# Optimization experiments

Hardware: AMD Instinct MI355X
Metric: run time of the kernel (lower is better)

The kernel has to match this reference:

```python
import jax, jax.numpy as jnp
import numpy as np

B, L, H, NE, SPAN = 16, 2048, 768, 64, 4
EPS_COS = 1e-8   # torch cosine_similarity eps
EPS_STD = 1e-5   # std stabilizer from the module


def _linear_init(key, fan_in, fan_out):
    s = 1.0 / np.sqrt(fan_in)
    kw, kb = jax.random.split(key)
    w = jax.random.uniform(kw, (fan_in, fan_out), jnp.float32, -s, s)
    b = jax.random.uniform(kb, (fan_out,), jnp.float32, -s, s)
    return w, b


def setup_inputs() -> dict:
    key = jax.random.key(0)
    ks = jax.random.split(key, 6)
    w1, b1 = _linear_init(ks[0], 2 * H + 1, H)
    w2, b2 = _linear_init(ks[1], H, 512)
    w3, b3 = _linear_init(ks[2], 512, 256)
    w4, b4 = _linear_init(ks[3], 256, 2)
    x = jax.random.normal(ks[4], (B, L, H), jnp.float32)
    entity_starts = jax.random.randint(ks[5], (B, NE), 0, L - SPAN)
    threshold = jnp.float32(0.9)
    return dict(x=x, threshold=threshold,
                w1=w1, b1=b1, w2=w2, b2=b2, w3=w3, b3=b3, w4=w4, b4=b4,
                entity_starts=entity_starts)


def reference(x, threshold, w1, b1, w2, b2, w3, b3, w4, b4, entity_starts):
    # --- per-entity span max-pool (segment-max over x) ---
    # gather span tokens: [B, NE*SPAN] token indices into the L axis
    idx = (entity_starts[:, :, None] + jnp.arange(SPAN)).reshape(B, NE * SPAN)
    spans = jnp.take_along_axis(x, idx[:, :, None], axis=1)      # [B, NE*SPAN, H]
    emb = spans.reshape(B, NE, SPAN, H).max(axis=2)               # [B, NE, H]

    # --- pairwise cosine similarity per batch ---
    norm = jnp.maximum(jnp.linalg.norm(emb, axis=-1, keepdims=True), EPS_COS)
    n = emb / norm
    cos = jnp.einsum('bie,bje->bij', n, n)                        # [B, NE, NE]
    std = jnp.std(cos, axis=(1, 2), ddof=1, keepdims=True)        # torch .std() is unbiased
    sim = (cos - threshold) / (std + EPS_STD)
    sim = jnp.triu(sim, k=1)

    # --- all i<j pairs: [sim, emb_i, emb_j] ---
    iu, ju = np.triu_indices(NE, k=1)                             # static pair indices
    feats = jnp.concatenate(
        [sim[:, iu, ju, None], emb[:, iu, :], emb[:, ju, :]], axis=-1
    ).reshape(-1, 2 * H + 1)                                      # [B*P, 2H+1]

    # --- classifier MLP (dropout = identity at eval) ---
    h = jax.nn.relu(feats @ w1 + b1)
    h = jax.nn.relu(h @ w2 + b2)
    h = jax.nn.relu(h @ w3 + b3)
    logits = h @ w4 + b4                                          # [B*P, 2]
    return logits
```

## Files before the change

kernel.cpp:

```cpp
#include <hip/hip_runtime.h>
#include <cstdint>
#include <cstddef>

#define B_    16
#define L_    2048
#define H_    768
#define NE_   64
#define SPAN_ 4
#define NPAIR 2016
#define NROWS (B_ * NPAIR)

typedef __bf16 bf16_t;
typedef __bf16 bf16x8 __attribute__((ext_vector_type(8)));
typedef __bf16 bf16x4 __attribute__((ext_vector_type(4)));
typedef float  floatx4 __attribute__((ext_vector_type(4)));

#define AS1 __attribute__((address_space(1)))
#define AS3 __attribute__((address_space(3)))

#define OFF_EMBH   ((size_t)3145728)
#define OFF_NRMG   ((size_t)4718592)
#define OFF_SIM    ((size_t)8126464)
#define OFF_W1ABT  ((size_t)8255488)
#define OFF_W2T    ((size_t)10614784)
#define OFF_W3T    ((size_t)11401216)
#define OFF_C1     ((size_t)11663360)
#define OFF_H2     ((size_t)67500032)
#define OFF_FLAG   ((size_t)117045248)
#define OFF_CANON  ((size_t)117045504)

#define SWZ(colb, row) ((colb) ^ (((row) & 3) << 4))

__device__ inline bf16_t cvt_elem(const void* p, size_t i, int isf) {
  if (isf) return (bf16_t)(((const float*)p)[i]);
  return ((const bf16_t*)p)[i];
}

__global__ __launch_bounds__(1024) void prep_kernel(
    const unsigned short* __restrict__ xu,
    const void* __restrict__ xv, const int* __restrict__ starts,
    const void* __restrict__ w1, const void* __restrict__ w2,
    const void* __restrict__ w3, const void* __restrict__ b1,
    const void* __restrict__ b2, const void* __restrict__ b3,
    const void* __restrict__ w4, const void* __restrict__ b4,
    int* __restrict__ flagout,
    bf16_t* __restrict__ w1abT, bf16_t* __restrict__ w2T,
    bf16_t* __restrict__ w3T, bf16_t* __restrict__ canon,
    bf16_t* __restrict__ embh, bf16_t* __restrict__ nrm_g) {
  __shared__ bf16_t tile[64][65];
  __shared__ int tot[16];
  int blk = blockIdx.x;
  int t = threadIdx.x;

  {
    int bad = 0;
    for (int i = t; i < 4096; i += 1024) {
      int e = (xu[i] >> 7) & 0xFF;
      if (e > 133 || (e > 0 && e < 90)) bad++;
    }
    for (int off = 32; off > 0; off >>= 1) bad += __shfl_down(bad, off, 64);
    if ((t & 63) == 0) tot[t >> 6] = bad;
    __syncthreads();
  }
  int sumb = 0;
#pragma unroll
  for (int i = 0; i < 16; i++) sumb += tot[i];
  int isf = (sumb > 200) ? 1 : 0;
  __syncthreads();

  for (int u = blk; u < 481; u += 256) {
    if (u < 64) {
      int lane = t & 63;
      int entity = u * 16 + (t >> 6);
      int st = starts[entity];
      int b = entity >> 6;
      size_t off = ((size_t)(b * L_ + st)) * H_;
      int d0 = lane * 12;
      float pool[12];
      float ss = 0.f;
      if (isf) {
        const float* xp = (const float*)xv + off + d0;
#pragma unroll
        for (int k = 0; k < 3; k++) {
          floatx4 r0 = *(const floatx4*)(xp + k * 4);
          floatx4 r1 = *(const floatx4*)(xp + H_ + k * 4);
          floatx4 r2 = *(const floatx4*)(xp + 2 * H_ + k * 4);
          floatx4 r3 = *(const floatx4*)(xp + 3 * H_ + k * 4);
#pragma unroll
          for (int q = 0; q < 4; q++) {
            float v = fmaxf(fmaxf(r0[q], r1[q]), fmaxf(r2[q], r3[q]));
            pool[k * 4 + q] = v;
            ss += v * v;
          }
        }
      } else {
        const bf16_t* xp = (const bf16_t*)xv + off + d0;
#pragma unroll
        for (int k = 0; k < 3; k++) {
          bf16x4 r0 = *(const bf16x4*)(xp + k * 4);
          bf16x4 r1 = *(const bf16x4*)(xp + H_ + k * 4);
          bf16x4 r2 = *(const bf16x4*)(xp + 2 * H_ + k * 4);
          bf16x4 r3 = *(const bf16x4*)(xp + 3 * H_ + k * 4);
#pragma unroll
          for (int q = 0; q < 4; q++) {
            float v = fmaxf(fmaxf((float)r0[q], (float)r1[q]),
                            fmaxf((float)r2[q], (float)r3[q]));
            pool[k * 4 + q] = v;
            ss += v * v;
          }
        }
      }
#pragma unroll
      for (int d = 1; d < 64; d <<= 1) ss += __shfl_xor(ss, d, 64);
      float inv = 1.0f / fmaxf(sqrtf(ss), 1e-8f);
      size_t base = (size_t)entity * 768 + d0;
#pragma unroll
      for (int k = 0; k < 3; k++) {
        bf16x4 op, on;
#pragma unroll
        for (int q = 0; q < 4; q++) {
          op[q] = (bf16_t)pool[k * 4 + q];
          on[q] = (bf16_t)(pool[k * 4 + q] * inv);
        }
        *(bf16x4*)(embh + base + k * 4) = op;
        *(bf16x4*)(nrm_g + base + k * 4) = on;
      }
    } else if (u == 64) {
      if (t == 0) flagout[0] = isf;
      for (int idx = t; idx < 2818; idx += 1024) {
        if (idx < 768)       canon[idx] = cvt_elem(w1, idx, isf);
        else if (idx < 1536) canon[idx] = cvt_elem(b1, idx - 768, isf);
        else if (idx < 2048) canon[idx] = cvt_elem(b2, idx - 1536, isf);
        else if (idx < 2304) canon[idx] = cvt_elem(b3, idx - 2048, isf);
        else if (idx < 2816) canon[idx] = cvt_elem(w4, idx - 2304, isf);
        else                 canon[idx] = cvt_elem(b4, idx - 2816, isf);
      }
    } else {
      int tix = u - 65;
      const void* src; size_t srcoff; bf16_t* dst; int K, N;
      if (tix < 144)      { src = w1; srcoff = 768;               dst = w1abT;          K = 768; N = 768; }
      else if (tix < 288) { src = w1; srcoff = (size_t)769 * 768; dst = w1abT + 589824; K = 768; N = 768; tix -= 144; }
      else if (tix < 384) { src = w2; srcoff = 0;                 dst = w2T;            K = 768; N = 512; tix -= 288; }
      else                { src = w3; srcoff = 0;                 dst = w3T;            K = 512; N = 256; tix -= 384; }
      int tiles_k = K >> 6;
      int tn_t = tix / tiles_k, tk_t = tix - tn_t * tiles_k;
      int ty = t >> 6, tx = t & 63;
      __syncthreads();
#pragma unroll
      for (int p = 0; p < 4; p++) {
        int kk = tk_t * 64 + p * 16 + ty;
        int nn = tn_t * 64 + tx;
        tile[p * 16 + ty][tx] = cvt_elem(src, srcoff + (size_t)kk * N + nn, isf);
      }
      __syncthreads();
#pragma unroll
      for (int p = 0; p < 4; p++) {
        int nn = tn_t * 64 + p * 16 + ty;
        int kk = tk_t * 64 + tx;
        dst[(size_t)nn * K + kk] = tile[tx][p * 16 + ty];
      }
    }
  }
}

__global__ __launch_bounds__(256) void cosgemm1_kernel(
    const bf16_t* __restrict__ nrm_g, const bf16_t* __restrict__ embh,
    const bf16_t* __restrict__ w1abT, const int* __restrict__ flagp,
    const void* __restrict__ thr_ptr, float* __restrict__ simv,
    bf16_t* __restrict__ C1) {
  __shared__ __align__(16) char shb[98304];
  __shared__ float red1[4], red2[4];
  __shared__ float scale_s, thr_s;
  int blk = blockIdx.x;
  int t = threadIdx.x;
  int w = t >> 6, lane = t & 63;
  int quad = lane >> 4, l15 = lane & 15;

  if (blk < 16) {
    bf16_t* nrm = (bf16_t*)shb;
    int b = blk;
    const bf16_t* src = nrm_g + (size_t)b * 64 * 768;
    {
      int lr = t >> 2, c0 = (t & 3) * 192;
      for (int i = 0; i < 24; i++) {
        int col = c0 + i * 8;
        bf16x8 v = *(const bf16x8*)(src + lr * 768 + col);
        *(bf16x8*)((char*)nrm + ((lr * 1536 + col * 2) ^ ((lr & 7) << 4))) = v;
      }
    }
    __syncthreads();

    int rowA = w * 16 + l15;
    int xa = (rowA & 7) << 4;
    floatx4 acc[4] = {};
    for (int k0 = 0; k0 < 768; k0 += 32) {
      int cb = (k0 + quad * 8) * 2;
      bf16x8 aF = *(const bf16x8*)((char*)nrm + ((rowA * 1536 + cb) ^ xa));
#pragma unroll
      for (int tj = 0; tj < 4; tj++) {
        int rb = tj * 16 + l15;
        bf16x8 bF = *(const bf16x8*)((char*)nrm + ((rb * 1536 + cb) ^ ((rb & 7) << 4)));
        acc[tj] = __builtin_amdgcn_mfma_f32_16x16x32_bf16(aF, bF, acc[tj], 0, 0, 0);
      }
    }

    float s1 = 0.f, s2 = 0.f;
#pragma unroll
    for (int tj = 0; tj < 4; tj++)
#pragma unroll
      for (int r = 0; r < 4; r++) { s1 += acc[tj][r]; s2 += acc[tj][r] * acc[tj][r]; }
#pragma unroll
    for (int d = 1; d < 64; d <<= 1) {
      s1 += __shfl_xor(s1, d, 64);
      s2 += __shfl_xor(s2, d, 64);
    }
    if (lane == 0) { red1[w] = s1; red2[w] = s2; }
    __syncthreads();
    if (t == 0) {
      float S1 = red1[0] + red1[1] + red1[2] + red1[3];
      float S2 = red2[0] + red2[1] + red2[2] + red2[3];
      float mean = S1 * (1.0f / 4096.0f);
      float var = (S2 - 4096.0f * mean * mean) * (1.0f / 4095.0f);
      float sd = sqrtf(fmaxf(var, 0.f));
      scale_s = 1.0f / (sd + 1e-5f);
      thr_s = flagp[0] ? *(const float*)thr_ptr : (float)(*(const bf16_t*)thr_ptr);
    }
    __syncthreads();
    float sc = scale_s, th = thr_s;
#pragma unroll
    for (int tj = 0; tj < 4; tj++) {
      int j = tj * 16 + l15;
#pragma unroll
      for (int r = 0; r < 4; r++) {
        int i = w * 16 + quad * 4 + r;
        if (j > i) {
          int p = i * 63 - (i * (i - 1)) / 2 + (j - i - 1);
          simv[b * NPAIR + p] = (acc[tj][r] - th) * sc;
        }
      }
    }
    return;
  }

  const int K = 768, N = 1536;
  int bi = blk - 16;
  int bm = bi / 12, bn = bi - bm * 12;
  int wm = w >> 1, wn = w & 1;

  floatx4 acc[2][4] = {};
  const char* Abase = (const char*)(embh + (size_t)bm * 64 * K);
  const char* Bbase = (const char*)(w1abT + (size_t)bn * 128 * K);
  const int rowbytes = K * 2;

  {
    int fo = w * 1024 + lane * 16;
    int row = fo >> 6, colb = fo & 63;
    __builtin_amdgcn_global_load_lds(
        (AS1 char*)(Abase + (size_t)row * rowbytes + SWZ(colb, row)),
        (AS3 char*)(shb + w * 1024), 16, 0, 0);
  }
#pragma unroll
  for (int it = 0; it < 2; it++) {
    int fo = (w * 2 + it) * 1024 + lane * 16;
    int row = fo >> 6, colb = fo & 63;
    __builtin_amdgcn_global_load_lds(
        (AS1 char*)(Bbase + (size_t)row * rowbytes + SWZ(colb, row)),
        (AS3 char*)(shb + 8192 + (w * 2 + it) * 1024), 16, 0, 0);
  }
  __syncthreads();

  for (int kt = 0; kt < 24; ++kt) {
    int cur = kt & 1, nxt = cur ^ 1;
    if (kt < 23) {
      int k1 = (kt + 1) * 32;
      {
        int fo = w * 1024 + lane * 16;
        int row = fo >> 6, colb = fo & 63;
        __builtin_amdgcn_global_load_lds(
            (AS1 char*)(Abase + (size_t)row * rowbytes + k1 * 2 + SWZ(colb, row)),
            (AS3 char*)(shb + nxt * 4096 + w * 1024), 16, 0, 0);
      }
#pragma unroll
      for (int it = 0; it < 2; it++) {
        int fo = (w * 2 + it) * 1024 + lane * 16;
        int row = fo >> 6, colb = fo & 63;
        __builtin_amdgcn_global_load_lds(
            (AS1 char*)(Bbase + (size_t)row * rowbytes + k1 * 2 + SWZ(colb, row)),
            (AS3 char*)(shb + 8192 + nxt * 8192 + (w * 2 + it) * 1024), 16, 0, 0);
      }
    }

    const char* Ac = shb + cur * 4096;
    const char* Bc = shb + 8192 + cur * 8192;
    bf16x8 aF[2], bF[4];
#pragma unroll
    for (int tm = 0; tm < 2; tm++) {
      int ra = wm * 32 + tm * 16 + l15;
      aF[tm] = *((const bf16x8*)(Ac + ra * 64 + SWZ(quad * 16, ra)));
    }
#pragma unroll
    for (int tn = 0; tn < 4; tn++) {
      int rb = wn * 64 + tn * 16 + l15;
      bF[tn] = *((const bf16x8*)(Bc + rb * 64 + SWZ(quad * 16, rb)));
    }
#pragma unroll
    for (int tm = 0; tm < 2; tm++)
#pragma unroll
      for (int tn = 0; tn < 4; tn++)
        acc[tm][tn] = __builtin_amdgcn_mfma_f32_16x16x32_bf16(aF[tm], bF[tn], acc[tm][tn], 0, 0, 0);
    __syncthreads();
  }

#pragma unroll
  for (int tm = 0; tm < 2; tm++) {
    int grow0 = bm * 64 + wm * 32 + tm * 16 + quad * 4;
#pragma unroll
    for (int tn = 0; tn < 4; tn++) {
      int gcol = bn * 128 + wn * 64 + tn * 16 + l15;
#pragma unroll
      for (int r = 0; r < 4; r++)
        C1[(size_t)(grow0 + r) * N + gcol] = (bf16_t)acc[tm][tn][r];
    }
  }
}

__global__ __launch_bounds__(512, 4) void gemm2_fused_kernel(
    const bf16_t* __restrict__ C1, const float* __restrict__ sim,
    const bf16_t* __restrict__ w2T, const bf16_t* __restrict__ canon,
    bf16_t* __restrict__ h2) {
  __shared__ __align__(16) bf16_t Asm[2][128 * 40];
  __shared__ __align__(16) bf16_t Bsm[2][256 * 32];
  __shared__ int   rowI[128], rowJ[128];
  __shared__ float rowS[128];
  __shared__ bf16_t w1s[768], b1s[768];
  __shared__ float b2s[256];
  int bm = blockIdx.x, bn = blockIdx.y;
  int t = threadIdx.x;

  if (t < 128) {
    int r = bm * 128 + t;
    int b = r / NPAIR, p = r - b * NPAIR;
    int i = 0, rem = p;
    while (rem >= 63 - i) { rem -= 63 - i; i++; }
    rowI[t] = b * 64 + i;
    rowJ[t] = b * 64 + i + 1 + rem;
    rowS[t] = sim[r];
  }
  for (int c = t; c < 768; c += 512) { w1s[c] = canon[c]; b1s[c] = canon[768 + c]; }
  if (t < 256) b2s[t] = (float)canon[1536 + bn * 256 + t];
  __syncthreads();

  int w = t >> 6, lane = t & 63;
  int quad = lane >> 4, l15 = lane & 15;
  int wm = w >> 2, wn = w & 3;
  floatx4 acc[4][4] = {};

  const char* Bbase = (const char*)(w2T + (size_t)bn * 256 * 768);

  int arow = t >> 2;
  int acolc = (t & 3) * 8;
  const bf16_t* Ai = C1 + (size_t)rowI[arow] * 1536 + acolc;
  const bf16_t* Aj = C1 + (size_t)rowJ[arow] * 1536 + 768 + acolc;
  float s = rowS[arow];

  bf16x8 pi = *(const bf16x8*)(Ai);
  bf16x8 pj = *(const bf16x8*)(Aj);
#pragma unroll
  for (int it = 0; it < 2; it++) {
    int fo = w * 2048 + it * 1024 + lane * 16;
    int row = fo >> 6, colb = fo & 63;
    __builtin_amdgcn_global_load_lds(
        (AS1 char*)(Bbase + (size_t)row * 1536 + SWZ(colb, row)),
        (AS3 char*)((char*)&Bsm[0][0] + w * 2048 + it * 1024),
        16, 0, 0);
  }
  {
    const bf16x8 wv8 = *(const bf16x8*)(w1s + acolc);
    const bf16x8 bv8 = *(const bf16x8*)(b1s + acolc);
    bf16x8 o;
#pragma unroll
    for (int q = 0; q < 8; q++)
      o[q] = (bf16_t)fmaxf((float)pi[q] + (float)pj[q] + s * (float)wv8[q] + (float)bv8[q], 0.f);
    *(bf16x8*)(&Asm[0][arow * 40 + acolc]) = o;
  }
  pi = *(const bf16x8*)(Ai + 32);
  pj = *(const bf16x8*)(Aj + 32);
  __syncthreads();

  for (int kt = 0; kt < 24; ++kt) {
    int cur = kt & 1, nxt = cur ^ 1;
    if (kt < 23) {
      int k1 = (kt + 1) * 32;
      bf16x8 npi, npj;
      if (kt < 22) {
        int k2 = (kt + 2) * 32;
        npi = *(const bf16x8*)(Ai + k2);
        npj = *(const bf16x8*)(Aj + k2);
      }
#pragma unroll
      for (int it = 0; it < 2; it++) {
        int fo = w * 2048 + it * 1024 + lane * 16;
        int row = fo >> 6, colb = fo & 63;
        __builtin_amdgcn_global_load_lds(
            (AS1 char*)(Bbase + (size_t)row * 1536 + k1 * 2 + SWZ(colb, row)),
            (AS3 char*)((char*)&Bsm[nxt][0] + w * 2048 + it * 1024),
            16, 0, 0);
      }
      {
        const bf16x8 wv8 = *(const bf16x8*)(w1s + k1 + acolc);
        const bf16x8 bv8 = *(const bf16x8*)(b1s + k1 + acolc);
        bf16x8 o;
#pragma unroll
        for (int q = 0; q < 8; q++)
          o[q] = (bf16_t)fmaxf((float)pi[q] + (float)pj[q] + s * (float)wv8[q] + (float)bv8[q], 0.f);
        *(bf16x8*)(&Asm[nxt][arow * 40 + acolc]) = o;
      }
      if (kt < 22) { pi = npi; pj = npj; }
    }

    bf16x8 aF[4], bF[4];
#pragma unroll
    for (int tm = 0; tm < 4; tm++)
      aF[tm] = *((const bf16x8*)(&Asm[cur][(wm * 64 + tm * 16 + l15) * 40 + quad * 8]));
#pragma unroll
    for (int tn = 0; tn < 4; tn++) {
      int rb = wn * 64 + tn * 16 + l15;
      bF[tn] = *((const bf16x8*)((const char*)&Bsm[cur][0] + rb * 64 + SWZ(quad * 16, rb)));
    }
#pragma unroll
    for (int tm = 0; tm < 4; tm++)
#pragma unroll
      for (int tn = 0; tn < 4; tn++)
        acc[tm][tn] = __builtin_amdgcn_mfma_f32_16x16x32_bf16(aF[tm], bF[tn], acc[tm][tn], 0, 0, 0);
    __syncthreads();
  }

#pragma unroll
  for (int tm = 0; tm < 4; tm++) {
    int grow0 = bm * 128 + wm * 64 + tm * 16 + quad * 4;
#pragma unroll
    for (int tn = 0; tn < 4; tn++) {
      int lcol = wn * 64 + tn * 16 + l15;
      int gcol = bn * 256 + lcol;
#pragma unroll
      for (int r = 0; r < 4; r++) {
        float v = fmaxf(acc[tm][tn][r] + b2s[lcol], 0.f);
        h2[(size_t)(grow0 + r) * 512 + gcol] = (bf16_t)v;
      }
    }
  }
}

__global__ __launch_bounds__(256) void gemm3_fused_kernel(
    const bf16_t* __restrict__ h2, const bf16_t* __restrict__ w3T,
    const bf16_t* __restrict__ canon, const int* __restrict__ flagp,
    void* __restrict__ out) {
  __shared__ __align__(16) bf16_t Asm[2][64 * 32];
  __shared__ __align__(16) bf16_t Bsm[2][256 * 32];
  __shared__ float part[64][2][4];
  __shared__ float w4s[512];
  __shared__ float b3s[256];
  int bm = blockIdx.x;
  int t = threadIdx.x;
  int w = t >> 6, lane = t & 63;
  int quad = lane >> 4, l15 = lane & 15;

  w4s[t]       = (float)canon[2304 + t];
  w4s[256 + t] = (float)canon[2304 + 256 + t];
  b3s[t]       = (float)canon[2048 + t];

  floatx4 acc[4][4] = {};
  const char* Abase = (const char*)(h2 + (size_t)bm * 64 * 512);
  const char* Bbase = (const char*)w3T;

  {
    int fo = w * 1024 + lane * 16;
    int row = fo >> 6, colb = fo & 63;
    __builtin_amdgcn_global_load_lds(
        (AS1 char*)(Abase + (size_t)row * 1024 + SWZ(colb, row)),
        (AS3 char*)((char*)&Asm[0][0] + w * 1024),
        16, 0, 0);
  }
#pragma unroll
  for (int it = 0; it < 4; it++) {
    int fo = w * 4096 + it * 1024 + lane * 16;
    int row = fo >> 6, colb = fo & 63;
    __builtin_amdgcn_global_load_lds(
        (AS1 char*)(Bbase + (size_t)row * 1024 + SWZ(colb, row)),
        (AS3 char*)((char*)&Bsm[0][0] + w * 4096 + it * 1024),
        16, 0, 0);
  }
  __syncthreads();

  for (int kt = 0; kt < 16; ++kt) {
    int cur = kt & 1, nxt = cur ^ 1;
    if (kt < 15) {
      int k1 = (kt + 1) * 32;
      {
        int fo = w * 1024 + lane * 16;
        int row = fo >> 6, colb = fo & 63;
        __builtin_amdgcn_global_load_lds(
            (AS1 char*)(Abase + (size_t)row * 1024 + k1 * 2 + SWZ(colb, row)),
            (AS3 char*)((char*)&Asm[nxt][0] + w * 1024),
            16, 0, 0);
      }
#pragma unroll
      for (int it = 0; it < 4; it++) {
        int fo = w * 4096 + it * 1024 + lane * 16;
        int row = fo >> 6, colb = fo & 63;
        __builtin_amdgcn_global_load_lds(
            (AS1 char*)(Bbase + (size_t)row * 1024 + k1 * 2 + SWZ(colb, row)),
            (AS3 char*)((char*)&Bsm[nxt][0] + w * 4096 + it * 1024),
            16, 0, 0);
      }
    }

    bf16x8 aF[4], bF[4];
#pragma unroll
    for (int tm = 0; tm < 4; tm++) {
      int ra = tm * 16 + l15;
      aF[tm] = *((const bf16x8*)((const char*)&Asm[cur][0] + ra * 64 + SWZ(quad * 16, ra)));
    }
#pragma unroll
    for (int tn = 0; tn < 4; tn++) {
      int rb = w * 64 + tn * 16 + l15;
      bF[tn] = *((const bf16x8*)((const char*)&Bsm[cur][0] + rb * 64 + SWZ(quad * 16, rb)));
    }
#pragma unroll
    for (int tm = 0; tm < 4; tm++)
#pragma unroll
      for (int tn = 0; tn < 4; tn++)
        acc[tm][tn] = __builtin_amdgcn_mfma_f32_16x16x32_bf16(aF[tm], bF[tn], acc[tm][tn], 0, 0, 0);
    __syncthreads();
  }

#pragma unroll
  for (int tm = 0; tm < 4; tm++) {
#pragma unroll
    for (int reg = 0; reg < 4; reg++) {
      float p0 = 0.f, p1 = 0.f;
#pragma unroll
      for (int tn = 0; tn < 4; tn++) {
        int col = w * 64 + tn * 16 + l15;
        float v = fmaxf(acc[tm][tn][reg] + b3s[col], 0.f);
        p0 += v * w4s[col * 2];
        p1 += v * w4s[col * 2 + 1];
      }
#pragma unroll
      for (int d = 1; d < 16; d <<= 1) {
        p0 += __shfl_xor(p0, d, 64);
        p1 += __shfl_xor(p1, d, 64);
      }
      if (l15 == 0) {
        int r = tm * 16 + quad * 4 + reg;
        part[r][0][w] = p0;
        part[r][1][w] = p1;
      }
    }
  }
  __syncthreads();
  if (t < 128) {
    int r = t >> 1, c = t & 1;
    float v = part[r][c][0] + part[r][c][1] + part[r][c][2] + part[r][c][3]
            + (float)canon[2816 + c];
    size_t rg = (size_t)bm * 64 + r;
    if (flagp[0]) ((float*)out)[rg * 2 + c] = v;
    else          ((bf16_t*)out)[rg * 2 + c] = (bf16_t)v;
  }
}

extern "C" void kernel_launch(void* const* d_in, const int* in_sizes, int n_in,
                              void* d_out, int out_size, void* d_ws, size_t ws_size,
                              hipStream_t stream) {
  const void* x      = d_in[0];
  const void* thr    = d_in[1];
  const void* w1     = d_in[2];
  const void* b1     = d_in[3];
  const void* w2     = d_in[4];
  const void* b2     = d_in[5];
  const void* w3     = d_in[6];
  const void* b3     = d_in[7];
  const void* w4     = d_in[8];
  const void* b4     = d_in[9];
  const int*  starts = (const int*)d_in[10];

  char* ws = (char*)d_ws;
  bf16_t* embh  = (bf16_t*)(ws + OFF_EMBH);
  bf16_t* nrm_g = (bf16_t*)(ws + OFF_NRMG);
  float*  simv  = (float*)(ws + OFF_SIM);
  bf16_t* w1abT = (bf16_t*)(ws + OFF_W1ABT);
  bf16_t* w2T   = (bf16_t*)(ws + OFF_W2T);
  bf16_t* w3T   = (bf16_t*)(ws + OFF_W3T);
  bf16_t* C1    = (bf16_t*)(ws + OFF_C1);
  bf16_t* h2    = (bf16_t*)(ws + OFF_H2);
  int*    flag  = (int*)(ws + OFF_FLAG);
  bf16_t* canon = (bf16_t*)(ws + OFF_CANON);

  prep_kernel<<<256, 1024, 0, stream>>>(
      (const unsigned short*)x, x, starts,
      w1, w2, w3, b1, b2, b3, w4, b4,
      flag, w1abT, w2T, w3T, canon, embh, nrm_g);

  cosgemm1_kernel<<<208, 256, 0, stream>>>(nrm_g, embh, w1abT, flag, thr,
                                           simv, C1);

  {
    dim3 g(NROWS / 128, 2);
    gemm2_fused_kernel<<<g, 512, 0, stream>>>(C1, simv, w2T, canon, h2);
  }

  gemm3_fused_kernel<<<NROWS / 64, 256, 0, stream>>>(h2, w3T, canon, flag, d_out);
}
```

Measured before the change: 226.7 us.

## Triple-buffer B/A tiles in gemm2 and gemm3 with fine-grained vmcnt waits

Moves the gemm2 and gemm3 main loops from double to triple buffering of the LDS tiles loaded by global_load_lds, issuing loads two K-steps ahead. The full __syncthreads is replaced by raw s_barrier with explicit partial vmcnt/lgkmcnt waits, so loads stay in flight across iterations. The aim is to hide global memory latency behind the MFMA work. In exchange it uses more LDS, which may lower occupancy, and it relies on hand-counted vmcnt values. gemm2's main loop waits only on lgkmcnt and drains vmcnt just on the last step, so correctness there depends on this being sufficient for the async LDS loads.

New measurement: 224.2 us. No clear change (-1.1%).

```diff
diff --git a/kernel.cpp b/kernel.cpp
--- a/kernel.cpp
+++ b/kernel.cpp
@@ -329,7 +329,7 @@
     const bf16_t* __restrict__ w2T, const bf16_t* __restrict__ canon,
     bf16_t* __restrict__ h2) {
   __shared__ __align__(16) bf16_t Asm[2][128 * 40];
-  __shared__ __align__(16) bf16_t Bsm[2][256 * 32];
+  __shared__ __align__(16) bf16_t Bsm[3][256 * 32];
   __shared__ int   rowI[128], rowJ[128];
   __shared__ float rowS[128];
   __shared__ bf16_t w1s[768], b1s[768];
@@ -363,17 +363,21 @@
   const bf16_t* Aj = C1 + (size_t)rowJ[arow] * 1536 + 768 + acolc;
   float s = rowS[arow];
 
+#define G2_STAGE_B(sidx)                                                      \
+  {                                                                           \
+    _Pragma("unroll")                                                         \
+    for (int it = 0; it < 2; it++) {                                          \
+      int fo = w * 2048 + it * 1024 + lane * 16;                              \
+      int row = fo >> 6, colb = fo & 63;                                      \
+      __builtin_amdgcn_global_load_lds(                                       \
+          (AS1 char*)(Bbase + (size_t)row * 1536 + (sidx) * 64 + SWZ(colb, row)), \
+          (AS3 char*)((char*)&Bsm[(sidx) % 3][0] + w * 2048 + it * 1024),     \
+          16, 0, 0);                                                          \
+    }                                                                         \
+  }
+
   bf16x8 pi = *(const bf16x8*)(Ai);
   bf16x8 pj = *(const bf16x8*)(Aj);
-#pragma unroll
-  for (int it = 0; it < 2; it++) {
-    int fo = w * 2048 + it * 1024 + lane * 16;
-    int row = fo >> 6, colb = fo & 63;
-    __builtin_amdgcn_global_load_lds(
-        (AS1 char*)(Bbase + (size_t)row * 1536 + SWZ(colb, row)),
-        (AS3 char*)((char*)&Bsm[0][0] + w * 2048 + it * 1024),
-        16, 0, 0);
-  }
   {
     const bf16x8 wv8 = *(const bf16x8*)(w1s + acolc);
     const bf16x8 bv8 = *(const bf16x8*)(b1s + acolc);
@@ -383,57 +387,54 @@
       o[q] = (bf16_t)fmaxf((float)pi[q] + (float)pj[q] + s * (float)wv8[q] + (float)bv8[q], 0.f);
     *(bf16x8*)(&Asm[0][arow * 40 + acolc]) = o;
   }
+  G2_STAGE_B(0);
   pi = *(const bf16x8*)(Ai + 32);
   pj = *(const bf16x8*)(Aj + 32);
-  __syncthreads();
-
+  G2_STAGE_B(1);
+  asm volatile("s_waitcnt lgkmcnt(0)" ::: "memory");
+  __builtin_amdgcn_sched_barrier(0);
+  __builtin_amdgcn_s_barrier();
+
+  bf16x8 npi, npj;
   for (int kt = 0; kt < 24; ++kt) {
-    int cur = kt & 1, nxt = cur ^ 1;
-    if (kt < 23) {
-      int k1 = (kt + 1) * 32;
-      bf16x8 npi, npj;
-      if (kt < 22) {
-        int k2 = (kt + 2) * 32;
-        npi = *(const bf16x8*)(Ai + k2);
-        npj = *(const bf16x8*)(Aj + k2);
-      }
-#pragma unroll
-      for (int it = 0; it < 2; it++) {
-        int fo = w * 2048 + it * 1024 + lane * 16;
-        int row = fo >> 6, colb = fo & 63;
-        __builtin_amdgcn_global_load_lds(
-            (AS1 char*)(Bbase + (size_t)row * 1536 + k1 * 2 + SWZ(colb, row)),
-            (AS3 char*)((char*)&Bsm[nxt][0] + w * 2048 + it * 1024),
-            16, 0, 0);
-      }
-      {
-        const bf16x8 wv8 = *(const bf16x8*)(w1s + k1 + acolc);
-        const bf16x8 bv8 = *(const bf16x8*)(b1s + k1 + acolc);
-        bf16x8 o;
-#pragma unroll
-        for (int q = 0; q < 8; q++)
-          o[q] = (bf16_t)fmaxf((float)pi[q] + (float)pj[q] + s * (float)wv8[q] + (float)bv8[q], 0.f);
-        *(bf16x8*)(&Asm[nxt][arow * 40 + acolc]) = o;
-      }
-      if (kt < 22) { pi = npi; pj = npj; }
-    }
+    if (kt + 2 < 24) {
+      int s2 = kt + 2;
+      npi = *(const bf16x8*)(Ai + s2 * 32);
+      npj = *(const bf16x8*)(Aj + s2 * 32);
+      G2_STAGE_B(s2);
+    }
+    if (kt + 1 < 24) {
+      const bf16x8 wv8 = *(const bf16x8*)(w1s + (kt + 1) * 32 + acolc);
+      const bf16x8 bv8 = *(const bf16x8*)(b1s + (kt + 1) * 32 + acolc);
+      bf16x8 o;
+#pragma unroll
+      for (int q = 0; q < 8; q++)
+        o[q] = (bf16_t)fmaxf((float)pi[q] + (float)pj[q] + s * (float)wv8[q] + (float)bv8[q], 0.f);
+      *(bf16x8*)(&Asm[(kt + 1) & 1][arow * 40 + acolc]) = o;
+      pi = npi; pj = npj;
+    }
+    asm volatile("s_waitcnt lgkmcnt(0)" ::: "memory");
+    if (kt == 23) asm volatile("s_waitcnt vmcnt(0)" ::: "memory");
+    __builtin_amdgcn_sched_barrier(0);
+    __builtin_amdgcn_s_barrier();
 
     bf16x8 aF[4], bF[4];
 #pragma unroll
     for (int tm = 0; tm < 4; tm++)
-      aF[tm] = *((const bf16x8*)(&Asm[cur][(wm * 64 + tm * 16 + l15) * 40 + quad * 8]));
+      aF[tm] = *((const bf16x8*)(&Asm[kt & 1][(wm * 64 + tm * 16 + l15) * 40 + quad * 8]));
 #pragma unroll
     for (int tn = 0; tn < 4; tn++) {
       int rb = wn * 64 + tn * 16 + l15;
-      bF[tn] = *((const bf16x8*)((const char*)&Bsm[cur][0] + rb * 64 + SWZ(quad * 16, rb)));
+      bF[tn] = *((const bf16x8*)((const char*)&Bsm[kt % 3][0] + rb * 64 + SWZ(quad * 16, rb)));
     }
 #pragma unroll
     for (int tm = 0; tm < 4; tm++)
 #pragma unroll
       for (int tn = 0; tn < 4; tn++)
         acc[tm][tn] = __builtin_amdgcn_mfma_f32_16x16x32_bf16(aF[tm], bF[tn], acc[tm][tn], 0, 0, 0);
-    __syncthreads();
-  }
+    __builtin_amdgcn_s_barrier();
+  }
+#undef G2_STAGE_B
 
 #pragma unroll
   for (int tm = 0; tm < 4; tm++) {
@@ -455,8 +456,8 @@
     const bf16_t* __restrict__ h2, const bf16_t* __restrict__ w3T,
     const bf16_t* __restrict__ canon, const int* __restrict__ flagp,
     void* __restrict__ out) {
-  __shared__ __align__(16) bf16_t Asm[2][64 * 32];
-  __shared__ __align__(16) bf16_t Bsm[2][256 * 32];
+  __shared__ __align__(16) bf16_t Asm[3][64 * 32];
+  __shared__ __align__(16) bf16_t Bsm[3][256 * 32];
   __shared__ float part[64][2][4];
   __shared__ float w4s[512];
   __shared__ float b3s[256];
@@ -468,71 +469,65 @@
   w4s[t]       = (float)canon[2304 + t];
   w4s[256 + t] = (float)canon[2304 + 256 + t];
   b3s[t]       = (float)canon[2048 + t];
+  __syncthreads();
 
   floatx4 acc[4][4] = {};
   const char* Abase = (const char*)(h2 + (size_t)bm * 64 * 512);
   const char* Bbase = (const char*)w3T;
 
-  {
-    int fo = w * 1024 + lane * 16;
-    int row = fo >> 6, colb = fo & 63;
-    __builtin_amdgcn_global_load_lds(
-        (AS1 char*)(Abase + (size_t)row * 1024 + SWZ(colb, row)),
-        (AS3 char*)((char*)&Asm[0][0] + w * 1024),
-        16, 0, 0);
-  }
-#pragma unroll
-  for (int it = 0; it < 4; it++) {
-    int fo = w * 4096 + it * 1024 + lane * 16;
-    int row = fo >> 6, colb = fo & 63;
-    __builtin_amdgcn_global_load_lds(
-        (AS1 char*)(Bbase + (size_t)row * 1024 + SWZ(colb, row)),
-        (AS3 char*)((char*)&Bsm[0][0] + w * 4096 + it * 1024),
-        16, 0, 0);
-  }
-  __syncthreads();
+#define G3_STAGE(sidx)                                                        \
+  {                                                                           \
+    {                                                                         \
+      int fo = w * 1024 + lane * 16;                                          \
+      int row = fo >> 6, colb = fo & 63;                                      \
+      __builtin_amdgcn_global_load_lds(                                       \
+          (AS1 char*)(Abase + (size_t)row * 1024 + (sidx) * 64 + SWZ(colb, row)), \
+          (AS3 char*)((char*)&Asm[(sidx) % 3][0] + w * 1024), 16, 0, 0);      \
+    }                                                                         \
+    _Pragma("unroll")                                                         \
+    for (int it = 0; it < 4; it++) {                                          \
+      int fo = w * 4096 + it * 1024 + lane * 16;                              \
+      int row = fo >> 6, colb = fo & 63;                                      \
+      __builtin_amdgcn_global_load_lds(                                       \
+          (AS1 char*)(Bbase + (size_t)row * 1024 + (sidx) * 64 + SWZ(colb, row)), \
+          (AS3 char*)((char*)&Bsm[(sidx) % 3][0] + w * 4096 + it * 1024),     \
+          16, 0, 0);                                                          \
+    }                                                                         \
+  }
+
+  G3_STAGE(0);
+  G3_STAGE(1);
+  asm volatile("s_waitcnt vmcnt(5)" ::: "memory");
+  __builtin_amdgcn_sched_barrier(0);
+  __builtin_amdgcn_s_barrier();
 
   for (int kt = 0; kt < 16; ++kt) {
-    int cur = kt & 1, nxt = cur ^ 1;
-    if (kt < 15) {
-      int k1 = (kt + 1) * 32;
-      {
-        int fo = w * 1024 + lane * 16;
-        int row = fo >> 6, colb = fo & 63;
-        __builtin_amdgcn_global_load_lds(
-            (AS1 char*)(Abase + (size_t)row * 1024 + k1 * 2 + SWZ(colb, row)),
-            (AS3 char*)((char*)&Asm[nxt][0] + w * 1024),
-            16, 0, 0);
-      }
-#pragma unroll
-      for (int it = 0; it < 4; it++) {
-        int fo = w * 4096 + it * 1024 + lane * 16;
-        int row = fo >> 6, colb = fo & 63;
-        __builtin_amdgcn_global_load_lds(
-            (AS1 char*)(Bbase + (size_t)row * 1024 + k1 * 2 + SWZ(colb, row)),
-            (AS3 char*)((char*)&Bsm[nxt][0] + w * 4096 + it * 1024),
-            16, 0, 0);
-      }
-    }
+    if (kt + 2 < 16) G3_STAGE(kt + 2);
+    if (kt < 14)       asm volatile("s_waitcnt vmcnt(10)" ::: "memory");
+    else if (kt == 14) asm volatile("s_waitcnt vmcnt(5)" ::: "memory");
+    else               asm volatile("s_waitcnt vmcnt(0)" ::: "memory");
+    __builtin_amdgcn_sched_barrier(0);
+    __builtin_amdgcn_s_barrier();
 
     bf16x8 aF[4], bF[4];
 #pragma unroll
     for (int tm = 0; tm < 4; tm++) {
       int ra = tm * 16 + l15;
-      aF[tm] = *((const bf16x8*)((const char*)&Asm[cur][0] + ra * 64 + SWZ(quad * 16, ra)));
+      aF[tm] = *((const bf16x8*)((const char*)&Asm[kt % 3][0] + ra * 64 + SWZ(quad * 16, ra)));
     }
 #pragma unroll
     for (int tn = 0; tn < 4; tn++) {
       int rb = w * 64 + tn * 16 + l15;
-      bF[tn] = *((const bf16x8*)((const char*)&Bsm[cur][0] + rb * 64 + SWZ(quad * 16, rb)));
+      bF[tn] = *((const bf16x8*)((const char*)&Bsm[kt % 3][0] + rb * 64 + SWZ(quad * 16, rb)));
     }
 #pragma unroll
     for (int tm = 0; tm < 4; tm++)
 #pragma unroll
       for (int tn = 0; tn < 4; tn++)
         acc[tm][tn] = __builtin_amdgcn_mfma_f32_16x16x32_bf16(aF[tm], bF[tn], acc[tm][tn], 0, 0, 0);
-    __syncthreads();
-  }
+    __builtin_amdgcn_s_barrier();
+  }
+#undef G3_STAGE
 
 #pragma unroll
   for (int tm = 0; tm < 4; tm++) {
```
